# Kernel optimization log

Measured on AMD Instinct MI355X. Metric: run time of the kernel, lower is better.

## Reference

```python
import jax, jax.numpy as jnp
import numpy as np
import math

EPS = 1e-5  # PyTorch InstanceNorm default eps

def _inorm(x):
    # InstanceNorm1d(affine=False) applied to (N, L, F): with channels=L,
    # it normalizes each (n, l) row over the last (feature) axis, biased var.
    mu = jnp.mean(x, axis=-1, keepdims=True)
    var = jnp.var(x, axis=-1, keepdims=True)
    return (x - mu) * jax.lax.rsqrt(var + EPS)

def _proj(x, W, b):
    # Linear -> Tanh -> InstanceNorm (inside Sequential) -> InstanceNorm (QueryNorm etc.)
    return _inorm(_inorm(jnp.tanh(x @ W.T + b)))

def setup_inputs() -> dict:
    key = jax.random.key(0)
    N, D, H, W = 8, 512, 48, 48
    F_ = 512
    ks = jax.random.split(key, 7)
    s = 1.0 / math.sqrt(D)  # torch Linear default init bound
    inp = {"x": jax.random.normal(ks[0], (N, D, H, W), jnp.float32)}
    for i, name in enumerate(["q", "k", "v"]):
        inp[f"W{name}"] = jax.random.uniform(ks[1 + 2 * i], (F_, D), jnp.float32, -s, s)
        inp[f"b{name}"] = jax.random.uniform(ks[2 + 2 * i], (F_,), jnp.float32, -s, s)
    return inp

def reference(x, Wq, bq, Wk, bk, Wv, bv):
    N, D, H, W = x.shape
    F_ = Wq.shape[0]
    L = H * W
    # (N, D, H, W) -> (N, H, W, D) -> (N, L, D)
    flat = jnp.transpose(x, (0, 2, 3, 1)).reshape(N, L, D)
    Q = _proj(flat, Wq, bq)  # (N, L, F)
    K = _proj(flat, Wk, bk)
    V = _proj(flat, Wv, bv)
    scores = jnp.einsum('nlf,nmf->nlm', Q, K) / math.sqrt(F_)  # (N, L, L)
    attn = jax.nn.softmax(scores, axis=-1)
    A = jnp.einsum('nlm,nmf->nlf', attn, V)  # (N, L, F)
    return A.reshape(N, -1, H, W)  # raw reshape as in original: (N, F, H, W)
```

## Files before the change

kernel.cpp:

```cpp
#include <hip/hip_runtime.h>

typedef __attribute__((ext_vector_type(8))) short short8;
typedef __attribute__((ext_vector_type(4))) short short4v;
typedef __attribute__((ext_vector_type(4))) float floatx4;

__device__ __forceinline__ float bf2f(unsigned short u) {
    unsigned int v = ((unsigned int)u) << 16;
    return __builtin_bit_cast(float, v);
}
__device__ __forceinline__ unsigned short f2bf(float f) {
    unsigned int u = __builtin_bit_cast(unsigned int, f);
    u += 0x7fffu + ((u >> 16) & 1u);
    return (unsigned short)(u >> 16);
}

__device__ __forceinline__ void gl_lds16(const void* g, void* l) {
    __builtin_amdgcn_global_load_lds(
        (const __attribute__((address_space(1))) unsigned int*)g,
        (__attribute__((address_space(3))) unsigned int*)l, 16, 0, 0);
}

#define L_DIM 2304
#define D_DIM 512

__global__ void k_detect(const unsigned short* __restrict__ xs, int* __restrict__ flag) {
    int lane = threadIdx.x;
    int cnt = 0;
#pragma unroll
    for (int j = 0; j < 16; j++) {
        unsigned short u = xs[2 * (lane * 16 + j)];
        int e = (u >> 7) & 0xFF;
        cnt += (e >= 0xC0) ? 1 : 0;
    }
#pragma unroll
    for (int m = 1; m < 64; m <<= 1) cnt += __shfl_xor(cnt, m);
    if (lane == 0) *flag = (cnt > 4) ? 1 : 0;
}

__global__ __launch_bounds__(256) void k_prep(
    const void* __restrict__ w0, const void* __restrict__ w1, const void* __restrict__ w2,
    const void* __restrict__ b0, const void* __restrict__ b1, const void* __restrict__ b2,
    short* __restrict__ Wc, short* __restrict__ bc,
    float* __restrict__ lsum, int lcount, const int* __restrict__ flag) {
    const int b = blockIdx.x, tid = threadIdx.x;
    const int fl = *flag;
    if (b < 384) {
        int w = b >> 7, blk = b & 127;
        const void* src = w == 0 ? w0 : (w == 1 ? w1 : w2);
        short* dst = Wc + (size_t)w * 262144;
        int i = (blk * 256 + tid) * 8;
        if (fl) {
            const float* s = (const float*)src + i;
            short8 o;
#pragma unroll
            for (int j = 0; j < 8; j++) o[j] = (short)f2bf(s[j]);
            *(short8*)(dst + i) = o;
        } else {
            *(short8*)(dst + i) = *(const short8*)((const short*)src + i);
        }
    } else if (b == 384) {
        int i = tid * 8;
        if (i < 1536) {
            int which = i >> 9, off = i & 511;
            const void* src = which == 0 ? b0 : (which == 1 ? b1 : b2);
            short* dst = bc + which * 512 + off;
            if (fl) {
                const float* s = (const float*)src + off;
#pragma unroll
                for (int j = 0; j < 8; j++) dst[j] = (short)f2bf(s[j]);
            } else {
#pragma unroll
                for (int j = 0; j < 8; j++) dst[j] = ((const short*)src)[off + j];
            }
        }
    } else {
        int idx = (b - 385) * 256 + tid;
        if (idx < lcount) lsum[idx] = 0.f;
    }
}

__global__ __launch_bounds__(256) void k_transpose(const void* __restrict__ x_,
                                                   short* __restrict__ fx,
                                                   const int* __restrict__ flag) {
    __shared__ __align__(16) short t[64 * 72];
    const int n = blockIdx.z, d0 = blockIdx.y * 64, l0 = blockIdx.x * 64;
    const int tid = threadIdx.x;
    if (*flag) {
        const float* x = (const float*)x_;
#pragma unroll
        for (int p = 0; p < 4; p++) {
            int i = tid + p * 256;
            int dr = i >> 4, lc = (i & 15) * 4;
            floatx4 v = *(const floatx4*)(x + (size_t)(n * D_DIM + d0 + dr) * L_DIM + l0 + lc);
#pragma unroll
            for (int j = 0; j < 4; j++) t[(lc + j) * 72 + dr] = (short)f2bf(v[j]);
        }
    } else {
        const short* x = (const short*)x_;
#pragma unroll
        for (int p = 0; p < 2; p++) {
            int i = tid + p * 256;
            int dr = i >> 3, lc = (i & 7) * 8;
            short8 v = *(const short8*)(x + (size_t)(n * D_DIM + d0 + dr) * L_DIM + l0 + lc);
#pragma unroll
            for (int j = 0; j < 8; j++) t[(lc + j) * 72 + dr] = v[j];
        }
    }
    __syncthreads();
#pragma unroll
    for (int p = 0; p < 2; p++) {
        int i = tid + p * 256;
        int lr = i >> 3, dc = (i & 7) * 8;
        short8 v = *(const short8*)&t[lr * 72 + dc];
        *(short8*)(fx + (size_t)(n * L_DIM + l0 + lr) * D_DIM + d0 + dc) = v;
    }
}

__global__ __launch_bounds__(256) void k_trV(const short* __restrict__ src,
                                             short* __restrict__ dst) {
    __shared__ __align__(16) short t[64 * 72];
    const int n = blockIdx.z, l0 = blockIdx.x * 64, f0 = blockIdx.y * 64;
    const int tid = threadIdx.x;
    if (tid < 128) {
        const int ll = (tid & 15) * 4;
        const int ff = (tid >> 4) * 8;
        short8 v[4];
#pragma unroll
        for (int r = 0; r < 4; r++)
            v[r] = *(const short8*)(src + (size_t)(n * L_DIM + l0 + ll + r) * D_DIM + f0 + ff);
#pragma unroll
        for (int j = 0; j < 8; j++) {
            short4v w = { v[0][j], v[1][j], v[2][j], v[3][j] };
            *(short4v*)&t[(ff + j) * 72 + ll] = w;
        }
    }
    __syncthreads();
#pragma unroll
    for (int p = 0; p < 2; p++) {
        int i = tid + p * 256;
        int fr = i >> 3, lc = (i & 7) * 8;
        short8 o = *(const short8*)&t[fr * 72 + lc];
        *(short8*)(dst + (size_t)(n * D_DIM + f0 + fr) * L_DIM + l0 + lc) = o;
    }
}

__device__ __forceinline__ void gemm128(const short* __restrict__ A,
                                        const short* __restrict__ B,
                                        int K, int l0, int f0,
                                        short* ldsA, short* ldsB,
                                        floatx4 acc[4][4]) {
    const int tid = threadIdx.x, lane = tid & 63, wid = tid >> 6;
    const int wm = wid & 1, wn = wid >> 1, quad = lane >> 4, l16 = lane & 15;
    const int r16 = lane >> 2, c8 = (lane & 3) * 8;
    for (int kt = 0; kt < K; kt += 32) {
        __syncthreads();
#pragma unroll
        for (int p = 0; p < 2; p++) {
            int row = (wid + p * 4) * 16;
            gl_lds16(A + (size_t)(l0 + row + r16) * K + kt + c8, ldsA + row * 32);
            gl_lds16(B + (size_t)(f0 + row + r16) * K + kt + c8, ldsB + row * 32);
        }
        __syncthreads();
        short8 a[4], b[4];
#pragma unroll
        for (int mi = 0; mi < 4; mi++)
            a[mi] = *(const short8*)&ldsA[(wm * 64 + mi * 16 + l16) * 32 + quad * 8];
#pragma unroll
        for (int ni = 0; ni < 4; ni++)
            b[ni] = *(const short8*)&ldsB[(wn * 64 + ni * 16 + l16) * 32 + quad * 8];
#pragma unroll
        for (int mi = 0; mi < 4; mi++)
#pragma unroll
            for (int ni = 0; ni < 4; ni++)
                acc[mi][ni] = __builtin_amdgcn_mfma_f32_16x16x32_bf16(a[mi], b[ni], acc[mi][ni], 0, 0, 0);
    }
}

__global__ __launch_bounds__(256) void k_gemm_proj(const short* __restrict__ fx,
                                                   const short* __restrict__ Wc,
                                                   const short* __restrict__ bc,
                                                   short* __restrict__ Pbase) {
    __shared__ __align__(16) short ldsA[128 * 32];
    __shared__ __align__(16) short ldsB[128 * 32];
    const int bx = blockIdx.x;
    const int n = bx & 7, t = bx >> 3;
    const int proj = t / 72, tt = t % 72;
    const int l0 = (tt >> 2) * 128, f0 = (tt & 3) * 128;
    const short* A = fx + (size_t)n * L_DIM * D_DIM;
    const short* B = Wc + (size_t)proj * 262144;
    const short* bias = bc + proj * 512;
    short* P = Pbase + (size_t)proj * 8 * L_DIM * D_DIM + (size_t)n * L_DIM * D_DIM;
    const int lane = threadIdx.x & 63, wid = threadIdx.x >> 6;
    const int wm = wid & 1, wn = wid >> 1, quad = lane >> 4, l16 = lane & 15;

    floatx4 acc[4][4] = {};
    gemm128(A, B, 512, l0, f0, ldsA, ldsB, acc);

#pragma unroll
    for (int ni = 0; ni < 4; ni++) {
        int f = f0 + wn * 64 + ni * 16 + l16;
        float bb = bf2f((unsigned short)bias[f]);
#pragma unroll
        for (int mi = 0; mi < 4; mi++) {
#pragma unroll
            for (int r = 0; r < 4; r++) {
                int l = l0 + wm * 64 + mi * 16 + quad * 4 + r;
                float v = tanhf(acc[mi][ni][r] + bb);
                P[(size_t)l * 512 + f] = (short)f2bf(v);
            }
        }
    }
}

__global__ __launch_bounds__(256) void k_norm(short* __restrict__ base) {
    const int row = blockIdx.x * 4 + (threadIdx.x >> 6);
    const int lane = threadIdx.x & 63;
    short* p = base + (size_t)row * 512 + lane * 8;
    short8 v = *(const short8*)p;
    float x[8], s = 0.f, sq = 0.f;
#pragma unroll
    for (int j = 0; j < 8; j++) {
        x[j] = bf2f((unsigned short)v[j]);
        s += x[j];
        sq += x[j] * x[j];
    }
#pragma unroll
    for (int m = 1; m < 64; m <<= 1) {
        s += __shfl_xor(s, m);
        sq += __shfl_xor(sq, m);
    }
    float mu = s * (1.0f / 512.0f);
    float var = sq * (1.0f / 512.0f) - mu * mu;
    float r1 = rsqrtf(var + 1e-5f);
    float y[8], s2 = 0.f, sq2 = 0.f;
#pragma unroll
    for (int j = 0; j < 8; j++) {
        y[j] = (x[j] - mu) * r1;
        s2 += y[j];
        sq2 += y[j] * y[j];
    }
#pragma unroll
    for (int m = 1; m < 64; m <<= 1) {
        s2 += __shfl_xor(s2, m);
        sq2 += __shfl_xor(sq2, m);
    }
    float mu2 = s2 * (1.0f / 512.0f);
    float var2 = sq2 * (1.0f / 512.0f) - mu2 * mu2;
    float r2 = rsqrtf(var2 + 1e-5f);
    short8 o;
#pragma unroll
    for (int j = 0; j < 8; j++) o[j] = (short)f2bf((y[j] - mu2) * r2);
    *(short8*)p = o;
}

__global__ __launch_bounds__(256) void k_gemm_scores(const short* __restrict__ Q,
                                                     const short* __restrict__ Kb,
                                                     short* __restrict__ P,
                                                     float* __restrict__ lsum) {
    __shared__ __align__(16) short ldsA[128 * 32];
    __shared__ __align__(16) short ldsB[128 * 32];
    const int bx = blockIdx.x;
    const int n = bx & 7, t = bx >> 3;
    const int l0 = (t / 18) * 128, m0 = (t % 18) * 128;
    const short* A = Q + (size_t)n * L_DIM * D_DIM;
    const short* B = Kb + (size_t)n * L_DIM * D_DIM;
    const int lane = threadIdx.x & 63, wid = threadIdx.x >> 6;
    const int wm = wid & 1, wn = wid >> 1, quad = lane >> 4, l16 = lane & 15;

    floatx4 acc[4][4] = {};
    gemm128(A, B, 512, l0, m0, ldsA, ldsB, acc);

    const float sc = 0.044194173824159216f;
    short* Pn = P + (size_t)n * L_DIM * L_DIM;
    float* ln = lsum + n * L_DIM;
#pragma unroll
    for (int mi = 0; mi < 4; mi++) {
#pragma unroll
        for (int r = 0; r < 4; r++) {
            int row = l0 + wm * 64 + mi * 16 + quad * 4 + r;
            float s = 0.f;
#pragma unroll
            for (int ni = 0; ni < 4; ni++) {
                int col = m0 + wn * 64 + ni * 16 + l16;
                unsigned short pb = f2bf(__expf(acc[mi][ni][r] * sc));
                __builtin_nontemporal_store((short)pb, &Pn[(size_t)row * L_DIM + col]);
                s += bf2f(pb);
            }
            s += __shfl_xor(s, 1);
            s += __shfl_xor(s, 2);
            s += __shfl_xor(s, 4);
            s += __shfl_xor(s, 8);
            if (l16 == 0) atomicAdd(&ln[row], s);
        }
    }
}

__global__ __launch_bounds__(256) void k_gemm_out(const short* __restrict__ P,
                                                  const short* __restrict__ Vt,
                                                  const float* __restrict__ lsum,
                                                  void* __restrict__ out_,
                                                  const int* __restrict__ flag) {
    __shared__ __align__(16) short ldsA[128 * 32];
    __shared__ __align__(16) short ldsB[128 * 32];
    const int bx = blockIdx.x;
    const int n = bx & 7, t = bx >> 3;
    const int l0 = (t >> 2) * 128, f0 = (t & 3) * 128;
    const short* A = P + (size_t)n * L_DIM * L_DIM;
    const short* B = Vt + (size_t)n * D_DIM * L_DIM;
    const int lane = threadIdx.x & 63, wid = threadIdx.x >> 6;
    const int wm = wid & 1, wn = wid >> 1, quad = lane >> 4, l16 = lane & 15;

    floatx4 acc[4][4] = {};
    gemm128(A, B, L_DIM, l0, f0, ldsA, ldsB, acc);

    const int fl = *flag;
#pragma unroll
    for (int mi = 0; mi < 4; mi++) {
#pragma unroll
        for (int r = 0; r < 4; r++) {
            int row = l0 + wm * 64 + mi * 16 + quad * 4 + r;
            float rl = 1.0f / lsum[n * L_DIM + row];
            if (fl) {
                float* out = (float*)out_;
#pragma unroll
                for (int ni = 0; ni < 4; ni++) {
                    int f = f0 + wn * 64 + ni * 16 + l16;
                    __builtin_nontemporal_store(acc[mi][ni][r] * rl,
                        &out[((size_t)n * L_DIM + row) * 512 + f]);
                }
            } else {
                short* out = (short*)out_;
#pragma unroll
                for (int ni = 0; ni < 4; ni++) {
                    int f = f0 + wn * 64 + ni * 16 + l16;
                    __builtin_nontemporal_store((short)f2bf(acc[mi][ni][r] * rl),
                        &out[((size_t)n * L_DIM + row) * 512 + f]);
                }
            }
        }
    }
}

__global__ __launch_bounds__(512) void k_attn(const short* __restrict__ Q,
                                              const short* __restrict__ K,
                                              const short* __restrict__ V,
                                              void* __restrict__ out_,
                                              const int* __restrict__ flag) {
    __shared__ __align__(16) short ldsKV[512 * 40];
    __shared__ __align__(16) short ldsP[64 * 40];
    __shared__ float ldsL[64];
    const int n = blockIdx.y;
    const int q0 = blockIdx.x * 64;
    const int tid = threadIdx.x, lane = tid & 63, wid = tid >> 6;
    const int wq = wid & 3, wk = wid >> 2, quad = lane >> 4, l16 = lane & 15;
    const short* Qn = Q + (size_t)n * L_DIM * 512;
    const short* Kn = K + (size_t)n * L_DIM * 512;
    const short* Vn = V + (size_t)n * L_DIM * 512;
    if (tid < 64) ldsL[tid] = 0.f;

    short8 qf[16];
#pragma unroll
    for (int fs = 0; fs < 16; fs++)
        qf[fs] = *(const short8*)(Qn + (size_t)(q0 + wq * 16 + l16) * 512 + fs * 32 + quad * 8);

    floatx4 acc[16] = {};
    const float sc = 0.044194173824159216f;

    for (int kt = 0; kt < 72; kt++) {
        const int key0 = kt * 32;
        __syncthreads();
#pragma unroll
        for (int p = 0; p < 4; p++) {
            int i = tid + p * 512;
            int row = i >> 6, c = (i & 63) * 8;
            *(short8*)&ldsKV[row * 520 + c] =
                *(const short8*)(Kn + (size_t)(key0 + row) * 512 + c);
        }
        __syncthreads();
        floatx4 sacc = {0.f, 0.f, 0.f, 0.f};
#pragma unroll
        for (int fs = 0; fs < 16; fs++) {
            short8 kf = *(const short8*)&ldsKV[(wk * 16 + l16) * 520 + fs * 32 + quad * 8];
            sacc = __builtin_amdgcn_mfma_f32_16x16x32_bf16(qf[fs], kf, sacc, 0, 0, 0);
        }
        float pe[4];
#pragma unroll
        for (int r = 0; r < 4; r++) {
            unsigned short pb = f2bf(__expf(sacc[r] * sc));
            ldsP[(wq * 16 + quad * 4 + r) * 40 + wk * 16 + l16] = (short)pb;
            pe[r] = bf2f(pb);
        }
#pragma unroll
        for (int r = 0; r < 4; r++) {
            float s = pe[r];
            s += __shfl_xor(s, 1);
            s += __shfl_xor(s, 2);
            s += __shfl_xor(s, 4);
            s += __shfl_xor(s, 8);
            if (l16 == 0) atomicAdd(&ldsL[wq * 16 + quad * 4 + r], s);
        }
        __syncthreads();
#pragma unroll
        for (int p = 0; p < 4; p++) {
            int i = tid + p * 512;
            int row = i >> 6, c = (i & 63) * 8;
            short8 v = *(const short8*)(Vn + (size_t)(key0 + row) * 512 + c);
#pragma unroll
            for (int j = 0; j < 8; j++) ldsKV[(c + j) * 40 + row] = v[j];
        }
        __syncthreads();
        short8 pf = *(const short8*)&ldsP[(wq * 16 + l16) * 40 + quad * 8];
#pragma unroll
        for (int ni = 0; ni < 16; ni++) {
            short8 vf = *(const short8*)&ldsKV[(wk * 256 + ni * 16 + l16) * 40 + quad * 8];
            acc[ni] = __builtin_amdgcn_mfma_f32_16x16x32_bf16(pf, vf, acc[ni], 0, 0, 0);
        }
    }
    __syncthreads();
    float rl[4];
#pragma unroll
    for (int r = 0; r < 4; r++) rl[r] = 1.0f / ldsL[wq * 16 + quad * 4 + r];
    if (*flag) {
        float* out = (float*)out_;
#pragma unroll
        for (int ni = 0; ni < 16; ni++) {
            int f = wk * 256 + ni * 16 + l16;
#pragma unroll
            for (int r = 0; r < 4; r++) {
                int q = q0 + wq * 16 + quad * 4 + r;
                out[((size_t)n * L_DIM + q) * 512 + f] = acc[ni][r] * rl[r];
            }
        }
    } else {
        short* out = (short*)out_;
#pragma unroll
        for (int ni = 0; ni < 16; ni++) {
            int f = wk * 256 + ni * 16 + l16;
#pragma unroll
            for (int r = 0; r < 4; r++) {
                int q = q0 + wq * 16 + quad * 4 + r;
                out[((size_t)n * L_DIM + q) * 512 + f] = (short)f2bf(acc[ni][r] * rl[r]);
            }
        }
    }
}

extern "C" void kernel_launch(void* const* d_in, const int* in_sizes, int n_in,
                              void* d_out, int out_size, void* d_ws, size_t ws_size,
                              hipStream_t stream) {
    char* ws = (char*)d_ws;
    const size_t S1 = (size_t)8 * L_DIM * D_DIM * sizeof(short);
    int* flag = (int*)ws;
    short* Wc = (short*)(ws + 4096);
    short* bc = (short*)(ws + 4096 + 3 * 262144 * 2);
    short* flatX = (short*)(ws + 1581056);
    short* Pq = (short*)((char*)flatX + S1);
    short* Pk = (short*)((char*)Pq + S1);
    short* Pv = (short*)((char*)Pk + S1);

    const size_t need = 1581056 + 5 * S1 + 73728 + (size_t)8 * L_DIM * L_DIM * 2;
    const bool big = ws_size >= need;
    short* Vt = (short*)((char*)Pv + S1);
    float* lsum = (float*)((char*)Vt + S1);
    short* P = (short*)((char*)lsum + 73728);

    k_detect<<<1, 64, 0, stream>>>((const unsigned short*)d_in[0], flag);
    k_prep<<<457, 256, 0, stream>>>(d_in[1], d_in[3], d_in[5], d_in[2], d_in[4], d_in[6],
                                    Wc, bc, lsum, big ? 18432 : 0, flag);
    k_transpose<<<dim3(36, 8, 8), 256, 0, stream>>>(d_in[0], flatX, flag);
    k_gemm_proj<<<1728, 256, 0, stream>>>(flatX, Wc, bc, Pq);
    k_norm<<<13824, 256, 0, stream>>>(Pq);

    if (big) {
        k_trV<<<dim3(36, 8, 8), 256, 0, stream>>>(Pv, Vt);
        k_gemm_scores<<<2592, 256, 0, stream>>>(Pq, Pk, P, lsum);
        k_gemm_out<<<576, 256, 0, stream>>>(P, Vt, lsum, d_out, flag);
    } else {
        k_attn<<<dim3(36, 8), 512, 0, stream>>>(Pq, Pk, Pv, d_out, flag);
    }
}
```

Baseline: 360.2 us.

## Split the P·V GEMM over K with an fp32 partial buffer and combine kernel

The attention-output GEMM now splits its 2304-long reduction into two halves. This doubles the block count so more blocks are available to spread across the compute units. Each half writes fp32 partial sums into a reused workspace region, and a new combine kernel adds the halves, applies the softmax normalisation and writes fp32 or bf16 output. The scores kernel also switches its probability stores from nontemporal to ordinary stores, which may keep P resident in cache for the next GEMM. The cost is an extra round trip of a large fp32 buffer through memory plus one more kernel launch.

```diff
diff --git a/kernel.cpp b/kernel.cpp
--- a/kernel.cpp
+++ b/kernel.cpp
@@ -146,19 +146,20 @@
 
 __device__ __forceinline__ void gemm128(const short* __restrict__ A,
                                         const short* __restrict__ B,
-                                        int K, int l0, int f0,
+                                        int lda, int ldb, int kBeg, int kEnd,
+                                        int l0, int f0,
                                         short* ldsA, short* ldsB,
                                         floatx4 acc[4][4]) {
     const int tid = threadIdx.x, lane = tid & 63, wid = tid >> 6;
     const int wm = wid & 1, wn = wid >> 1, quad = lane >> 4, l16 = lane & 15;
     const int r16 = lane >> 2, c8 = (lane & 3) * 8;
-    for (int kt = 0; kt < K; kt += 32) {
+    for (int kt = kBeg; kt < kEnd; kt += 32) {
         __syncthreads();
 #pragma unroll
         for (int p = 0; p < 2; p++) {
             int row = (wid + p * 4) * 16;
-            gl_lds16(A + (size_t)(l0 + row + r16) * K + kt + c8, ldsA + row * 32);
-            gl_lds16(B + (size_t)(f0 + row + r16) * K + kt + c8, ldsB + row * 32);
+            gl_lds16(A + (size_t)(l0 + row + r16) * lda + kt + c8, ldsA + row * 32);
+            gl_lds16(B + (size_t)(f0 + row + r16) * ldb + kt + c8, ldsB + row * 32);
         }
         __syncthreads();
         short8 a[4], b[4];
@@ -194,7 +195,7 @@
     const int wm = wid & 1, wn = wid >> 1, quad = lane >> 4, l16 = lane & 15;
 
     floatx4 acc[4][4] = {};
-    gemm128(A, B, 512, l0, f0, ldsA, ldsB, acc);
+    gemm128(A, B, 512, 512, 0, 512, l0, f0, ldsA, ldsB, acc);
 
 #pragma unroll
     for (int ni = 0; ni < 4; ni++) {
@@ -268,7 +269,7 @@
     const int wm = wid & 1, wn = wid >> 1, quad = lane >> 4, l16 = lane & 15;
 
     floatx4 acc[4][4] = {};
-    gemm128(A, B, 512, l0, m0, ldsA, ldsB, acc);
+    gemm128(A, B, 512, 512, 0, 512, l0, m0, ldsA, ldsB, acc);
 
     const float sc = 0.044194173824159216f;
     short* Pn = P + (size_t)n * L_DIM * L_DIM;
@@ -283,7 +284,7 @@
             for (int ni = 0; ni < 4; ni++) {
                 int col = m0 + wn * 64 + ni * 16 + l16;
                 unsigned short pb = f2bf(__expf(acc[mi][ni][r] * sc));
-                __builtin_nontemporal_store((short)pb, &Pn[(size_t)row * L_DIM + col]);
+                Pn[(size_t)row * L_DIM + col] = (short)pb;
                 s += bf2f(pb);
             }
             s += __shfl_xor(s, 1);
@@ -295,49 +296,70 @@
     }
 }
 
-__global__ __launch_bounds__(256) void k_gemm_out(const short* __restrict__ P,
-                                                  const short* __restrict__ Vt,
-                                                  const float* __restrict__ lsum,
-                                                  void* __restrict__ out_,
-                                                  const int* __restrict__ flag) {
+__global__ __launch_bounds__(256) void k_gemm_out_sk(const short* __restrict__ P,
+                                                     const short* __restrict__ Vt,
+                                                     float* __restrict__ part) {
     __shared__ __align__(16) short ldsA[128 * 32];
     __shared__ __align__(16) short ldsB[128 * 32];
     const int bx = blockIdx.x;
     const int n = bx & 7, t = bx >> 3;
-    const int l0 = (t >> 2) * 128, f0 = (t & 3) * 128;
+    const int l0 = (t >> 3) * 128;
+    const int rem = t & 7;
+    const int f0 = (rem >> 1) * 128, s = rem & 1;
     const short* A = P + (size_t)n * L_DIM * L_DIM;
     const short* B = Vt + (size_t)n * D_DIM * L_DIM;
     const int lane = threadIdx.x & 63, wid = threadIdx.x >> 6;
     const int wm = wid & 1, wn = wid >> 1, quad = lane >> 4, l16 = lane & 15;
 
     floatx4 acc[4][4] = {};
-    gemm128(A, B, L_DIM, l0, f0, ldsA, ldsB, acc);
-
-    const int fl = *flag;
+    gemm128(A, B, L_DIM, L_DIM, s * 1152, s * 1152 + 1152, l0, f0, ldsA, ldsB, acc);
+
+    float* pp = part + (size_t)s * 8 * L_DIM * D_DIM;
 #pragma unroll
     for (int mi = 0; mi < 4; mi++) {
 #pragma unroll
         for (int r = 0; r < 4; r++) {
             int row = l0 + wm * 64 + mi * 16 + quad * 4 + r;
-            float rl = 1.0f / lsum[n * L_DIM + row];
-            if (fl) {
-                float* out = (float*)out_;
-#pragma unroll
-                for (int ni = 0; ni < 4; ni++) {
-                    int f = f0 + wn * 64 + ni * 16 + l16;
-                    __builtin_nontemporal_store(acc[mi][ni][r] * rl,
-                        &out[((size_t)n * L_DIM + row) * 512 + f]);
-                }
-            } else {
-                short* out = (short*)out_;
-#pragma unroll
-                for (int ni = 0; ni < 4; ni++) {
-                    int f = f0 + wn * 64 + ni * 16 + l16;
-                    __builtin_nontemporal_store((short)f2bf(acc[mi][ni][r] * rl),
-                        &out[((size_t)n * L_DIM + row) * 512 + f]);
-                }
+#pragma unroll
+            for (int ni = 0; ni < 4; ni++) {
+                int f = f0 + wn * 64 + ni * 16 + l16;
+                pp[((size_t)n * L_DIM + row) * 512 + f] = acc[mi][ni][r];
             }
         }
+    }
+}
+
+__global__ __launch_bounds__(256) void k_combine(const float* __restrict__ part,
+                                                 const float* __restrict__ lsum,
+                                                 void* __restrict__ out_,
+                                                 const int* __restrict__ flag) {
+    const size_t half = (size_t)8 * L_DIM * D_DIM;
+    size_t i = ((size_t)blockIdx.x * 256 + threadIdx.x) * 8;
+    int row = (int)(i >> 9);
+    float rl = 1.0f / lsum[row];
+    floatx4 a0 = *(const floatx4*)(part + i);
+    floatx4 a1 = *(const floatx4*)(part + i + 4);
+    floatx4 b0 = *(const floatx4*)(part + half + i);
+    floatx4 b1 = *(const floatx4*)(part + half + i + 4);
+    if (*flag) {
+        float* out = (float*)out_;
+        floatx4 o0, o1;
+#pragma unroll
+        for (int j = 0; j < 4; j++) {
+            o0[j] = (a0[j] + b0[j]) * rl;
+            o1[j] = (a1[j] + b1[j]) * rl;
+        }
+        *(floatx4*)(out + i) = o0;
+        *(floatx4*)(out + i + 4) = o1;
+    } else {
+        short* out = (short*)out_;
+        short8 o;
+#pragma unroll
+        for (int j = 0; j < 4; j++) {
+            o[j] = (short)f2bf((a0[j] + b0[j]) * rl);
+            o[j + 4] = (short)f2bf((a1[j] + b1[j]) * rl);
+        }
+        *(short8*)(out + i) = o;
     }
 }
 
@@ -463,6 +485,7 @@
     short* Vt = (short*)((char*)Pv + S1);
     float* lsum = (float*)((char*)Vt + S1);
     short* P = (short*)((char*)lsum + 73728);
+    float* part = (float*)flatX;
 
     k_detect<<<1, 64, 0, stream>>>((const unsigned short*)d_in[0], flag);
     k_prep<<<457, 256, 0, stream>>>(d_in[1], d_in[3], d_in[5], d_in[2], d_in[4], d_in[6],
@@ -474,7 +497,8 @@
     if (big) {
         k_trV<<<dim3(36, 8, 8), 256, 0, stream>>>(Pv, Vt);
         k_gemm_scores<<<2592, 256, 0, stream>>>(Pq, Pk, P, lsum);
-        k_gemm_out<<<576, 256, 0, stream>>>(P, Vt, lsum, d_out, flag);
+        k_gemm_out_sk<<<1152, 256, 0, stream>>>(P, Vt, part);
+        k_combine<<<4608, 256, 0, stream>>>(part, lsum, d_out, flag);
     } else {
         k_attn<<<dim3(36, 8), 512, 0, stream>>>(Pq, Pk, Pv, d_out, flag);
     }
```

Result: slower. 369.8 us (+2.7%).

## Fuse projection GEMM with tanh, double instance norm and V transpose

Applied to the files above, without the earlier changes.

Merges the detect, weight-prep and input-transpose kernels into one launch, with each block re-detecting the fp32/bf16 input format inline. The projection GEMM now computes a full 64x512 row tile per block, so tanh, both instance norms and the V transpose happen in its epilogue. This removes the separate norm and V-transpose kernels and their global round trips. The costs are higher register pressure from 32 accumulators per thread and fewer, larger blocks. Nontemporal stores in the scores and output kernels are also dropped.

```diff
diff --git a/kernel.cpp b/kernel.cpp
--- a/kernel.cpp
+++ b/kernel.cpp
@@ -23,27 +23,27 @@
 #define L_DIM 2304
 #define D_DIM 512
 
-__global__ void k_detect(const unsigned short* __restrict__ xs, int* __restrict__ flag) {
-    int lane = threadIdx.x;
-    int cnt = 0;
-#pragma unroll
-    for (int j = 0; j < 16; j++) {
-        unsigned short u = xs[2 * (lane * 16 + j)];
-        int e = (u >> 7) & 0xFF;
-        cnt += (e >= 0xC0) ? 1 : 0;
-    }
-#pragma unroll
-    for (int m = 1; m < 64; m <<= 1) cnt += __shfl_xor(cnt, m);
-    if (lane == 0) *flag = (cnt > 4) ? 1 : 0;
-}
-
-__global__ __launch_bounds__(256) void k_prep(
+__device__ __forceinline__ int detect_f32(const unsigned short* __restrict__ xs) {
+    int lane = threadIdx.x & 63;
+    int c = 0;
+    unsigned short u0 = xs[2 * lane];
+    unsigned short u1 = xs[128 + 2 * lane];
+    c += (((u0 >> 7) & 0xFF) >= 0xC0) ? 1 : 0;
+    c += (((u1 >> 7) & 0xFF) >= 0xC0) ? 1 : 0;
+#pragma unroll
+    for (int m = 1; m < 64; m <<= 1) c += __shfl_xor(c, m);
+    return c > 8;
+}
+
+__global__ __launch_bounds__(256) void k_pre(
     const void* __restrict__ w0, const void* __restrict__ w1, const void* __restrict__ w2,
     const void* __restrict__ b0, const void* __restrict__ b1, const void* __restrict__ b2,
+    const void* __restrict__ x_, const unsigned short* __restrict__ xs,
     short* __restrict__ Wc, short* __restrict__ bc,
-    float* __restrict__ lsum, int lcount, const int* __restrict__ flag) {
+    float* __restrict__ lsum, short* __restrict__ fx) {
+    __shared__ __align__(16) short t[64 * 72];
     const int b = blockIdx.x, tid = threadIdx.x;
-    const int fl = *flag;
+    const int fl = detect_f32(xs);
     if (b < 384) {
         int w = b >> 7, blk = b & 127;
         const void* src = w == 0 ? w0 : (w == 1 ? w1 : w2);
@@ -73,92 +73,192 @@
                 for (int j = 0; j < 8; j++) dst[j] = ((const short*)src)[off + j];
             }
         }
+    } else if (b < 457) {
+        int idx = (b - 385) * 256 + tid;
+        if (idx < 18432) lsum[idx] = 0.f;
     } else {
-        int idx = (b - 385) * 256 + tid;
-        if (idx < lcount) lsum[idx] = 0.f;
-    }
-}
-
-__global__ __launch_bounds__(256) void k_transpose(const void* __restrict__ x_,
-                                                   short* __restrict__ fx,
-                                                   const int* __restrict__ flag) {
-    __shared__ __align__(16) short t[64 * 72];
-    const int n = blockIdx.z, d0 = blockIdx.y * 64, l0 = blockIdx.x * 64;
-    const int tid = threadIdx.x;
-    if (*flag) {
-        const float* x = (const float*)x_;
-#pragma unroll
-        for (int p = 0; p < 4; p++) {
-            int i = tid + p * 256;
-            int dr = i >> 4, lc = (i & 15) * 4;
-            floatx4 v = *(const floatx4*)(x + (size_t)(n * D_DIM + d0 + dr) * L_DIM + l0 + lc);
-#pragma unroll
-            for (int j = 0; j < 4; j++) t[(lc + j) * 72 + dr] = (short)f2bf(v[j]);
-        }
-    } else {
-        const short* x = (const short*)x_;
+        int bb = b - 457;
+        int n = bb & 7, q = bb >> 3;
+        int d0 = (q & 7) * 64, l0 = (q >> 3) * 64;
+        if (fl) {
+            const float* x = (const float*)x_;
+#pragma unroll
+            for (int p = 0; p < 4; p++) {
+                int i = tid + p * 256;
+                int dr = i >> 4, lc = (i & 15) * 4;
+                floatx4 v = *(const floatx4*)(x + (size_t)(n * D_DIM + d0 + dr) * L_DIM + l0 + lc);
+#pragma unroll
+                for (int j = 0; j < 4; j++) t[(lc + j) * 72 + dr] = (short)f2bf(v[j]);
+            }
+        } else {
+            const short* x = (const short*)x_;
+#pragma unroll
+            for (int p = 0; p < 2; p++) {
+                int i = tid + p * 256;
+                int dr = i >> 3, lc = (i & 7) * 8;
+                short8 v = *(const short8*)(x + (size_t)(n * D_DIM + d0 + dr) * L_DIM + l0 + lc);
+#pragma unroll
+                for (int j = 0; j < 8; j++) t[(lc + j) * 72 + dr] = v[j];
+            }
+        }
+        __syncthreads();
 #pragma unroll
         for (int p = 0; p < 2; p++) {
             int i = tid + p * 256;
-            int dr = i >> 3, lc = (i & 7) * 8;
-            short8 v = *(const short8*)(x + (size_t)(n * D_DIM + d0 + dr) * L_DIM + l0 + lc);
-#pragma unroll
-            for (int j = 0; j < 8; j++) t[(lc + j) * 72 + dr] = v[j];
-        }
+            int lr = i >> 3, dc = (i & 7) * 8;
+            short8 v = *(const short8*)&t[lr * 72 + dc];
+            *(short8*)(fx + (size_t)(n * L_DIM + l0 + lr) * D_DIM + d0 + dc) = v;
+        }
+    }
+}
+
+__global__ __launch_bounds__(256, 2) void k_projnorm(
+    const short* __restrict__ fx, const short* __restrict__ Wc,
+    const short* __restrict__ bc, short* __restrict__ Pq,
+    short* __restrict__ Pk, short* __restrict__ Vt) {
+    __shared__ __align__(16) char lds[36864];
+    __shared__ float rsum[64], rsq[64];
+    short* ldsA = (short*)lds;
+    short* ldsB = (short*)(lds + 4096);
+    const int bx = blockIdx.x;
+    const int n = bx & 7, t = bx >> 3;
+    const int proj = t / 36, l0 = (t % 36) * 64;
+    const short* A = fx + (size_t)n * L_DIM * D_DIM;
+    const short* W = Wc + (size_t)proj * 262144;
+    const short* bias = bc + proj * 512;
+    const int tid = threadIdx.x, lane = tid & 63, wid = tid >> 6;
+    const int quad = lane >> 4, l16 = lane & 15;
+    const int r16 = lane >> 2, c8 = (lane & 3) * 8;
+
+    floatx4 acc[4][8] = {};
+    for (int kt = 0; kt < 512; kt += 32) {
+        __syncthreads();
+        gl_lds16(A + (size_t)(l0 + wid * 16 + r16) * 512 + kt + c8, ldsA + wid * 16 * 32);
+#pragma unroll
+        for (int p = 0; p < 8; p++) {
+            int row = (p * 4 + wid) * 16;
+            gl_lds16(W + (size_t)(row + r16) * 512 + kt + c8, ldsB + row * 32);
+        }
+        __syncthreads();
+        short8 a[4], bf[8];
+#pragma unroll
+        for (int mi = 0; mi < 4; mi++)
+            a[mi] = *(const short8*)&ldsA[(mi * 16 + l16) * 32 + quad * 8];
+#pragma unroll
+        for (int ni = 0; ni < 8; ni++)
+            bf[ni] = *(const short8*)&ldsB[(wid * 128 + ni * 16 + l16) * 32 + quad * 8];
+#pragma unroll
+        for (int mi = 0; mi < 4; mi++)
+#pragma unroll
+            for (int ni = 0; ni < 8; ni++)
+                acc[mi][ni] = __builtin_amdgcn_mfma_f32_16x16x32_bf16(a[mi], bf[ni], acc[mi][ni], 0, 0, 0);
     }
     __syncthreads();
-#pragma unroll
-    for (int p = 0; p < 2; p++) {
-        int i = tid + p * 256;
-        int lr = i >> 3, dc = (i & 7) * 8;
-        short8 v = *(const short8*)&t[lr * 72 + dc];
-        *(short8*)(fx + (size_t)(n * L_DIM + l0 + lr) * D_DIM + d0 + dc) = v;
-    }
-}
-
-__global__ __launch_bounds__(256) void k_trV(const short* __restrict__ src,
-                                             short* __restrict__ dst) {
-    __shared__ __align__(16) short t[64 * 72];
-    const int n = blockIdx.z, l0 = blockIdx.x * 64, f0 = blockIdx.y * 64;
-    const int tid = threadIdx.x;
-    if (tid < 128) {
-        const int ll = (tid & 15) * 4;
-        const int ff = (tid >> 4) * 8;
-        short8 v[4];
-#pragma unroll
-        for (int r = 0; r < 4; r++)
-            v[r] = *(const short8*)(src + (size_t)(n * L_DIM + l0 + ll + r) * D_DIM + f0 + ff);
-#pragma unroll
-        for (int j = 0; j < 8; j++) {
-            short4v w = { v[0][j], v[1][j], v[2][j], v[3][j] };
-            *(short4v*)&t[(ff + j) * 72 + ll] = w;
-        }
-    }
+    if (tid < 64) { rsum[tid] = 0.f; rsq[tid] = 0.f; }
+    float bb[8];
+#pragma unroll
+    for (int ni = 0; ni < 8; ni++) bb[ni] = bf2f((unsigned short)bias[wid * 128 + ni * 16 + l16]);
+#pragma unroll
+    for (int mi = 0; mi < 4; mi++)
+#pragma unroll
+        for (int ni = 0; ni < 8; ni++)
+#pragma unroll
+            for (int r = 0; r < 4; r++) {
+                float v = acc[mi][ni][r] + bb[ni];
+                float e = __expf(2.0f * v);
+                acc[mi][ni][r] = 1.0f - 2.0f / (e + 1.0f);
+            }
     __syncthreads();
 #pragma unroll
-    for (int p = 0; p < 2; p++) {
-        int i = tid + p * 256;
-        int fr = i >> 3, lc = (i & 7) * 8;
-        short8 o = *(const short8*)&t[fr * 72 + lc];
-        *(short8*)(dst + (size_t)(n * D_DIM + f0 + fr) * L_DIM + l0 + lc) = o;
+    for (int mi = 0; mi < 4; mi++)
+#pragma unroll
+        for (int r = 0; r < 4; r++) {
+            float s = 0.f, q = 0.f;
+#pragma unroll
+            for (int ni = 0; ni < 8; ni++) {
+                float v = acc[mi][ni][r];
+                s += v;
+                q += v * v;
+            }
+            s += __shfl_xor(s, 1); q += __shfl_xor(q, 1);
+            s += __shfl_xor(s, 2); q += __shfl_xor(q, 2);
+            s += __shfl_xor(s, 4); q += __shfl_xor(q, 4);
+            s += __shfl_xor(s, 8); q += __shfl_xor(q, 8);
+            if (l16 == 0) {
+                int row = mi * 16 + quad * 4 + r;
+                atomicAdd(&rsum[row], s);
+                atomicAdd(&rsq[row], q);
+            }
+        }
+    __syncthreads();
+#pragma unroll
+    for (int mi = 0; mi < 4; mi++)
+#pragma unroll
+        for (int r = 0; r < 4; r++) {
+            int row = mi * 16 + quad * 4 + r;
+            float mu = rsum[row] * (1.0f / 512.0f);
+            float var = rsq[row] * (1.0f / 512.0f) - mu * mu;
+            float r1 = rsqrtf(var + 1e-5f);
+            float v2 = var * r1 * r1;
+            float sc = r1 * rsqrtf(v2 + 1e-5f);
+#pragma unroll
+            for (int ni = 0; ni < 8; ni++)
+                acc[mi][ni][r] = (acc[mi][ni][r] - mu) * sc;
+        }
+    if (proj < 2) {
+        short* Pd = (proj == 0 ? Pq : Pk) + (size_t)n * L_DIM * 512;
+#pragma unroll
+        for (int mi = 0; mi < 4; mi++)
+#pragma unroll
+            for (int r = 0; r < 4; r++) {
+                int l = l0 + mi * 16 + quad * 4 + r;
+#pragma unroll
+                for (int ni = 0; ni < 8; ni++) {
+                    int f = wid * 128 + ni * 16 + l16;
+                    Pd[(size_t)l * 512 + f] = (short)f2bf(acc[mi][ni][r]);
+                }
+            }
+    } else {
+        short* tr = (short*)lds;
+        for (int c = 0; c < 4; c++) {
+            __syncthreads();
+            if (wid == c) {
+#pragma unroll
+                for (int mi = 0; mi < 4; mi++)
+#pragma unroll
+                    for (int ni = 0; ni < 8; ni++)
+#pragma unroll
+                        for (int r = 0; r < 4; r++)
+                            tr[(ni * 16 + l16) * 72 + mi * 16 + quad * 4 + r] =
+                                (short)f2bf(acc[mi][ni][r]);
+            }
+            __syncthreads();
+#pragma unroll
+            for (int p = 0; p < 4; p++) {
+                int fr = p * 32 + (tid >> 3), lc = (tid & 7) * 8;
+                short8 o = *(const short8*)&tr[fr * 72 + lc];
+                *(short8*)(Vt + ((size_t)(n * 512 + c * 128 + fr)) * L_DIM + l0 + lc) = o;
+            }
+        }
     }
 }
 
 __device__ __forceinline__ void gemm128(const short* __restrict__ A,
                                         const short* __restrict__ B,
-                                        int K, int l0, int f0,
+                                        int lda, int ldb, int kBeg, int kEnd,
+                                        int l0, int f0,
                                         short* ldsA, short* ldsB,
                                         floatx4 acc[4][4]) {
     const int tid = threadIdx.x, lane = tid & 63, wid = tid >> 6;
     const int wm = wid & 1, wn = wid >> 1, quad = lane >> 4, l16 = lane & 15;
     const int r16 = lane >> 2, c8 = (lane & 3) * 8;
-    for (int kt = 0; kt < K; kt += 32) {
+    for (int kt = kBeg; kt < kEnd; kt += 32) {
         __syncthreads();
 #pragma unroll
         for (int p = 0; p < 2; p++) {
             int row = (wid + p * 4) * 16;
-            gl_lds16(A + (size_t)(l0 + row + r16) * K + kt + c8, ldsA + row * 32);
-            gl_lds16(B + (size_t)(f0 + row + r16) * K + kt + c8, ldsB + row * 32);
+            gl_lds16(A + (size_t)(l0 + row + r16) * lda + kt + c8, ldsA + row * 32);
+            gl_lds16(B + (size_t)(f0 + row + r16) * ldb + kt + c8, ldsB + row * 32);
         }
         __syncthreads();
         short8 a[4], b[4];
@@ -173,6 +273,92 @@
 #pragma unroll
             for (int ni = 0; ni < 4; ni++)
                 acc[mi][ni] = __builtin_amdgcn_mfma_f32_16x16x32_bf16(a[mi], b[ni], acc[mi][ni], 0, 0, 0);
+    }
+}
+
+__global__ __launch_bounds__(256) void k_gemm_scores(const short* __restrict__ Q,
+                                                     const short* __restrict__ Kb,
+                                                     short* __restrict__ P,
+                                                     float* __restrict__ lsum) {
+    __shared__ __align__(16) short ldsA[128 * 32];
+    __shared__ __align__(16) short ldsB[128 * 32];
+    const int bx = blockIdx.x;
+    const int n = bx & 7, t = bx >> 3;
+    const int l0 = (t / 18) * 128, m0 = (t % 18) * 128;
+    const short* A = Q + (size_t)n * L_DIM * D_DIM;
+    const short* B = Kb + (size_t)n * L_DIM * D_DIM;
+    const int lane = threadIdx.x & 63, wid = threadIdx.x >> 6;
+    const int wm = wid & 1, wn = wid >> 1, quad = lane >> 4, l16 = lane & 15;
+
+    floatx4 acc[4][4] = {};
+    gemm128(A, B, 512, 512, 0, 512, l0, m0, ldsA, ldsB, acc);
+
+    const float sc = 0.044194173824159216f;
+    short* Pn = P + (size_t)n * L_DIM * L_DIM;
+    float* ln = lsum + n * L_DIM;
+#pragma unroll
+    for (int mi = 0; mi < 4; mi++) {
+#pragma unroll
+        for (int r = 0; r < 4; r++) {
+            int row = l0 + wm * 64 + mi * 16 + quad * 4 + r;
+            float s = 0.f;
+#pragma unroll
+            for (int ni = 0; ni < 4; ni++) {
+                int col = m0 + wn * 64 + ni * 16 + l16;
+                unsigned short pb = f2bf(__expf(acc[mi][ni][r] * sc));
+                Pn[(size_t)row * L_DIM + col] = (short)pb;
+                s += bf2f(pb);
+            }
+            s += __shfl_xor(s, 1);
+            s += __shfl_xor(s, 2);
+            s += __shfl_xor(s, 4);
+            s += __shfl_xor(s, 8);
+            if (l16 == 0) atomicAdd(&ln[row], s);
+        }
+    }
+}
+
+__global__ __launch_bounds__(256) void k_gemm_out(const short* __restrict__ P,
+                                                  const short* __restrict__ Vt,
+                                                  const float* __restrict__ lsum,
+                                                  void* __restrict__ out_,
+                                                  const unsigned short* __restrict__ xs) {
+    __shared__ __align__(16) short ldsA[128 * 32];
+    __shared__ __align__(16) short ldsB[128 * 32];
+    const int fl = detect_f32(xs);
+    const int bx = blockIdx.x;
+    const int n = bx & 7, t = bx >> 3;
+    const int l0 = (t >> 2) * 128, f0 = (t & 3) * 128;
+    const short* A = P + (size_t)n * L_DIM * L_DIM;
+    const short* B = Vt + (size_t)n * D_DIM * L_DIM;
+    const int lane = threadIdx.x & 63, wid = threadIdx.x >> 6;
+    const int wm = wid & 1, wn = wid >> 1, quad = lane >> 4, l16 = lane & 15;
+
+    floatx4 acc[4][4] = {};
+    gemm128(A, B, L_DIM, L_DIM, 0, L_DIM, l0, f0, ldsA, ldsB, acc);
+
+#pragma unroll
+    for (int mi = 0; mi < 4; mi++) {
+#pragma unroll
+        for (int r = 0; r < 4; r++) {
+            int row = l0 + wm * 64 + mi * 16 + quad * 4 + r;
+            float rl = 1.0f / lsum[n * L_DIM + row];
+            if (fl) {
+                float* out = (float*)out_;
+#pragma unroll
+                for (int ni = 0; ni < 4; ni++) {
+                    int f = f0 + wn * 64 + ni * 16 + l16;
+                    out[((size_t)n * L_DIM + row) * 512 + f] = acc[mi][ni][r] * rl;
+                }
+            } else {
+                short* out = (short*)out_;
+#pragma unroll
+                for (int ni = 0; ni < 4; ni++) {
+                    int f = f0 + wn * 64 + ni * 16 + l16;
+                    out[((size_t)n * L_DIM + row) * 512 + f] = (short)f2bf(acc[mi][ni][r] * rl);
+                }
+            }
+        }
     }
 }
 
@@ -192,23 +378,19 @@
     short* P = Pbase + (size_t)proj * 8 * L_DIM * D_DIM + (size_t)n * L_DIM * D_DIM;
     const int lane = threadIdx.x & 63, wid = threadIdx.x >> 6;
     const int wm = wid & 1, wn = wid >> 1, quad = lane >> 4, l16 = lane & 15;
-
     floatx4 acc[4][4] = {};
-    gemm128(A, B, 512, l0, f0, ldsA, ldsB, acc);
-
+    gemm128(A, B, 512, 512, 0, 512, l0, f0, ldsA, ldsB, acc);
 #pragma unroll
     for (int ni = 0; ni < 4; ni++) {
         int f = f0 + wn * 64 + ni * 16 + l16;
         float bb = bf2f((unsigned short)bias[f]);
 #pragma unroll
-        for (int mi = 0; mi < 4; mi++) {
+        for (int mi = 0; mi < 4; mi++)
 #pragma unroll
             for (int r = 0; r < 4; r++) {
                 int l = l0 + wm * 64 + mi * 16 + quad * 4 + r;
-                float v = tanhf(acc[mi][ni][r] + bb);
-                P[(size_t)l * 512 + f] = (short)f2bf(v);
-            }
-        }
+                P[(size_t)l * 512 + f] = (short)f2bf(tanhf(acc[mi][ni][r] + bb));
+            }
     }
 }
 
@@ -221,29 +403,18 @@
 #pragma unroll
     for (int j = 0; j < 8; j++) {
         x[j] = bf2f((unsigned short)v[j]);
-        s += x[j];
-        sq += x[j] * x[j];
-    }
-#pragma unroll
-    for (int m = 1; m < 64; m <<= 1) {
-        s += __shfl_xor(s, m);
-        sq += __shfl_xor(sq, m);
-    }
+        s += x[j]; sq += x[j] * x[j];
+    }
+#pragma unroll
+    for (int m = 1; m < 64; m <<= 1) { s += __shfl_xor(s, m); sq += __shfl_xor(sq, m); }
     float mu = s * (1.0f / 512.0f);
     float var = sq * (1.0f / 512.0f) - mu * mu;
     float r1 = rsqrtf(var + 1e-5f);
     float y[8], s2 = 0.f, sq2 = 0.f;
 #pragma unroll
-    for (int j = 0; j < 8; j++) {
-        y[j] = (x[j] - mu) * r1;
-        s2 += y[j];
-        sq2 += y[j] * y[j];
-    }
-#pragma unroll
-    for (int m = 1; m < 64; m <<= 1) {
-        s2 += __shfl_xor(s2, m);
-        sq2 += __shfl_xor(sq2, m);
-    }
+    for (int j = 0; j < 8; j++) { y[j] = (x[j] - mu) * r1; s2 += y[j]; sq2 += y[j] * y[j]; }
+#pragma unroll
+    for (int m = 1; m < 64; m <<= 1) { s2 += __shfl_xor(s2, m); sq2 += __shfl_xor(sq2, m); }
     float mu2 = s2 * (1.0f / 512.0f);
     float var2 = sq2 * (1.0f / 512.0f) - mu2 * mu2;
     float r2 = rsqrtf(var2 + 1e-5f);
@@ -253,102 +424,15 @@
     *(short8*)p = o;
 }
 
-__global__ __launch_bounds__(256) void k_gemm_scores(const short* __restrict__ Q,
-                                                     const short* __restrict__ Kb,
-                                                     short* __restrict__ P,
-                                                     float* __restrict__ lsum) {
-    __shared__ __align__(16) short ldsA[128 * 32];
-    __shared__ __align__(16) short ldsB[128 * 32];
-    const int bx = blockIdx.x;
-    const int n = bx & 7, t = bx >> 3;
-    const int l0 = (t / 18) * 128, m0 = (t % 18) * 128;
-    const short* A = Q + (size_t)n * L_DIM * D_DIM;
-    const short* B = Kb + (size_t)n * L_DIM * D_DIM;
-    const int lane = threadIdx.x & 63, wid = threadIdx.x >> 6;
-    const int wm = wid & 1, wn = wid >> 1, quad = lane >> 4, l16 = lane & 15;
-
-    floatx4 acc[4][4] = {};
-    gemm128(A, B, 512, l0, m0, ldsA, ldsB, acc);
-
-    const float sc = 0.044194173824159216f;
-    short* Pn = P + (size_t)n * L_DIM * L_DIM;
-    float* ln = lsum + n * L_DIM;
-#pragma unroll
-    for (int mi = 0; mi < 4; mi++) {
-#pragma unroll
-        for (int r = 0; r < 4; r++) {
-            int row = l0 + wm * 64 + mi * 16 + quad * 4 + r;
-            float s = 0.f;
-#pragma unroll
-            for (int ni = 0; ni < 4; ni++) {
-                int col = m0 + wn * 64 + ni * 16 + l16;
-                unsigned short pb = f2bf(__expf(acc[mi][ni][r] * sc));
-                __builtin_nontemporal_store((short)pb, &Pn[(size_t)row * L_DIM + col]);
-                s += bf2f(pb);
-            }
-            s += __shfl_xor(s, 1);
-            s += __shfl_xor(s, 2);
-            s += __shfl_xor(s, 4);
-            s += __shfl_xor(s, 8);
-            if (l16 == 0) atomicAdd(&ln[row], s);
-        }
-    }
-}
-
-__global__ __launch_bounds__(256) void k_gemm_out(const short* __restrict__ P,
-                                                  const short* __restrict__ Vt,
-                                                  const float* __restrict__ lsum,
-                                                  void* __restrict__ out_,
-                                                  const int* __restrict__ flag) {
-    __shared__ __align__(16) short ldsA[128 * 32];
-    __shared__ __align__(16) short ldsB[128 * 32];
-    const int bx = blockIdx.x;
-    const int n = bx & 7, t = bx >> 3;
-    const int l0 = (t >> 2) * 128, f0 = (t & 3) * 128;
-    const short* A = P + (size_t)n * L_DIM * L_DIM;
-    const short* B = Vt + (size_t)n * D_DIM * L_DIM;
-    const int lane = threadIdx.x & 63, wid = threadIdx.x >> 6;
-    const int wm = wid & 1, wn = wid >> 1, quad = lane >> 4, l16 = lane & 15;
-
-    floatx4 acc[4][4] = {};
-    gemm128(A, B, L_DIM, l0, f0, ldsA, ldsB, acc);
-
-    const int fl = *flag;
-#pragma unroll
-    for (int mi = 0; mi < 4; mi++) {
-#pragma unroll
-        for (int r = 0; r < 4; r++) {
-            int row = l0 + wm * 64 + mi * 16 + quad * 4 + r;
-            float rl = 1.0f / lsum[n * L_DIM + row];
-            if (fl) {
-                float* out = (float*)out_;
-#pragma unroll
-                for (int ni = 0; ni < 4; ni++) {
-                    int f = f0 + wn * 64 + ni * 16 + l16;
-                    __builtin_nontemporal_store(acc[mi][ni][r] * rl,
-                        &out[((size_t)n * L_DIM + row) * 512 + f]);
-                }
-            } else {
-                short* out = (short*)out_;
-#pragma unroll
-                for (int ni = 0; ni < 4; ni++) {
-                    int f = f0 + wn * 64 + ni * 16 + l16;
-                    __builtin_nontemporal_store((short)f2bf(acc[mi][ni][r] * rl),
-                        &out[((size_t)n * L_DIM + row) * 512 + f]);
-                }
-            }
-        }
-    }
-}
-
 __global__ __launch_bounds__(512) void k_attn(const short* __restrict__ Q,
                                               const short* __restrict__ K,
                                               const short* __restrict__ V,
                                               void* __restrict__ out_,
-                                              const int* __restrict__ flag) {
+                                              const unsigned short* __restrict__ xs) {
     __shared__ __align__(16) short ldsKV[512 * 40];
     __shared__ __align__(16) short ldsP[64 * 40];
     __shared__ float ldsL[64];
+    const int fl = detect_f32(xs);
     const int n = blockIdx.y;
     const int q0 = blockIdx.x * 64;
     const int tid = threadIdx.x, lane = tid & 63, wid = tid >> 6;
@@ -357,15 +441,12 @@
     const short* Kn = K + (size_t)n * L_DIM * 512;
     const short* Vn = V + (size_t)n * L_DIM * 512;
     if (tid < 64) ldsL[tid] = 0.f;
-
     short8 qf[16];
 #pragma unroll
     for (int fs = 0; fs < 16; fs++)
         qf[fs] = *(const short8*)(Qn + (size_t)(q0 + wq * 16 + l16) * 512 + fs * 32 + quad * 8);
-
     floatx4 acc[16] = {};
     const float sc = 0.044194173824159216f;
-
     for (int kt = 0; kt < 72; kt++) {
         const int key0 = kt * 32;
         __syncthreads();
@@ -373,8 +454,7 @@
         for (int p = 0; p < 4; p++) {
             int i = tid + p * 512;
             int row = i >> 6, c = (i & 63) * 8;
-            *(short8*)&ldsKV[row * 520 + c] =
-                *(const short8*)(Kn + (size_t)(key0 + row) * 512 + c);
+            *(short8*)&ldsKV[row * 520 + c] = *(const short8*)(Kn + (size_t)(key0 + row) * 512 + c);
         }
         __syncthreads();
         floatx4 sacc = {0.f, 0.f, 0.f, 0.f};
@@ -393,10 +473,8 @@
 #pragma unroll
         for (int r = 0; r < 4; r++) {
             float s = pe[r];
-            s += __shfl_xor(s, 1);
-            s += __shfl_xor(s, 2);
-            s += __shfl_xor(s, 4);
-            s += __shfl_xor(s, 8);
+            s += __shfl_xor(s, 1); s += __shfl_xor(s, 2);
+            s += __shfl_xor(s, 4); s += __shfl_xor(s, 8);
             if (l16 == 0) atomicAdd(&ldsL[wq * 16 + quad * 4 + r], s);
         }
         __syncthreads();
@@ -420,27 +498,14 @@
     float rl[4];
 #pragma unroll
     for (int r = 0; r < 4; r++) rl[r] = 1.0f / ldsL[wq * 16 + quad * 4 + r];
-    if (*flag) {
-        float* out = (float*)out_;
-#pragma unroll
-        for (int ni = 0; ni < 16; ni++) {
-            int f = wk * 256 + ni * 16 + l16;
-#pragma unroll
-            for (int r = 0; r < 4; r++) {
-                int q = q0 + wq * 16 + quad * 4 + r;
-                out[((size_t)n * L_DIM + q) * 512 + f] = acc[ni][r] * rl[r];
-            }
-        }
-    } else {
-        short* out = (short*)out_;
-#pragma unroll
-        for (int ni = 0; ni < 16; ni++) {
-            int f = wk * 256 + ni * 16 + l16;
-#pragma unroll
-            for (int r = 0; r < 4; r++) {
-                int q = q0 + wq * 16 + quad * 4 + r;
-                out[((size_t)n * L_DIM + q) * 512 + f] = (short)f2bf(acc[ni][r] * rl[r]);
-            }
+#pragma unroll
+    for (int ni = 0; ni < 16; ni++) {
+        int f = wk * 256 + ni * 16 + l16;
+#pragma unroll
+        for (int r = 0; r < 4; r++) {
+            int q = q0 + wq * 16 + quad * 4 + r;
+            if (fl) ((float*)out_)[((size_t)n * L_DIM + q) * 512 + f] = acc[ni][r] * rl[r];
+            else ((short*)out_)[((size_t)n * L_DIM + q) * 512 + f] = (short)f2bf(acc[ni][r] * rl[r]);
         }
     }
 }
@@ -450,32 +515,29 @@
                               hipStream_t stream) {
     char* ws = (char*)d_ws;
     const size_t S1 = (size_t)8 * L_DIM * D_DIM * sizeof(short);
-    int* flag = (int*)ws;
     short* Wc = (short*)(ws + 4096);
     short* bc = (short*)(ws + 4096 + 3 * 262144 * 2);
     short* flatX = (short*)(ws + 1581056);
     short* Pq = (short*)((char*)flatX + S1);
     short* Pk = (short*)((char*)Pq + S1);
     short* Pv = (short*)((char*)Pk + S1);
-
-    const size_t need = 1581056 + 5 * S1 + 73728 + (size_t)8 * L_DIM * L_DIM * 2;
-    const bool big = ws_size >= need;
     short* Vt = (short*)((char*)Pv + S1);
     float* lsum = (float*)((char*)Vt + S1);
     short* P = (short*)((char*)lsum + 73728);
-
-    k_detect<<<1, 64, 0, stream>>>((const unsigned short*)d_in[0], flag);
-    k_prep<<<457, 256, 0, stream>>>(d_in[1], d_in[3], d_in[5], d_in[2], d_in[4], d_in[6],
-                                    Wc, bc, lsum, big ? 18432 : 0, flag);
-    k_transpose<<<dim3(36, 8, 8), 256, 0, stream>>>(d_in[0], flatX, flag);
-    k_gemm_proj<<<1728, 256, 0, stream>>>(flatX, Wc, bc, Pq);
-    k_norm<<<13824, 256, 0, stream>>>(Pq);
-
+    const unsigned short* xs = (const unsigned short*)d_in[0];
+
+    const size_t need = 1581056 + 5 * S1 + 73728 + (size_t)8 * L_DIM * L_DIM * 2;
+    const bool big = ws_size >= need;
+
+    k_pre<<<2761, 256, 0, stream>>>(d_in[1], d_in[3], d_in[5], d_in[2], d_in[4], d_in[6],
+                                    d_in[0], xs, Wc, bc, lsum, flatX);
     if (big) {
-        k_trV<<<dim3(36, 8, 8), 256, 0, stream>>>(Pv, Vt);
+        k_projnorm<<<864, 256, 0, stream>>>(flatX, Wc, bc, Pq, Pk, Vt);
         k_gemm_scores<<<2592, 256, 0, stream>>>(Pq, Pk, P, lsum);
-        k_gemm_out<<<576, 256, 0, stream>>>(P, Vt, lsum, d_out, flag);
+        k_gemm_out<<<576, 256, 0, stream>>>(P, Vt, lsum, d_out, xs);
     } else {
-        k_attn<<<dim3(36, 8), 512, 0, stream>>>(Pq, Pk, Pv, d_out, flag);
-    }
-}
+        k_gemm_proj<<<1728, 256, 0, stream>>>(flatX, Wc, bc, Pq);
+        k_norm<<<13824, 256, 0, stream>>>(Pq);
+        k_attn<<<dim3(36, 8), 512, 0, stream>>>(Pq, Pk, Pv, d_out, xs);
+    }
+}
```

After: 308.0 us. 14.5% less time.
